# Performance work log

Hardware: AMD Instinct MI355X
Metric: run time of the kernel (lower is better)

Reference implementation:

```python
import jax, jax.numpy as jnp
import numpy as np

DIM = 512
HEADS = 8
HEAD_DIM = DIM // HEADS
SCALE = HEAD_DIM ** -0.5
B, N = 256, 144


def setup_inputs() -> dict:
    key = jax.random.key(0)
    k1, k2, k3, k4, k5, k6 = jax.random.split(key, 6)
    x = jax.random.normal(k1, (B, N, DIM), dtype=jnp.float32)
    topo_all_fea = jax.random.normal(k2, (B, N, DIM), dtype=jnp.float32)
    # nn.Linear weights stored as [out, in]
    kv_w = jax.random.normal(k3, (2 * DIM, DIM), dtype=jnp.float32) * 0.02
    q_w = jax.random.normal(k4, (DIM, DIM), dtype=jnp.float32) * 0.02
    proj_w = jax.random.normal(k5, (DIM, DIM), dtype=jnp.float32) * 0.02
    proj_b = jax.random.normal(k6, (DIM,), dtype=jnp.float32) * 0.02
    return {"x": x, "topo_all_fea": topo_all_fea, "kv_w": kv_w,
            "q_w": q_w, "proj_w": proj_w, "proj_b": proj_b, "is_end": 1}


def reference(x, topo_all_fea, kv_w, q_w, proj_w, proj_b, is_end):
    # block_pos == 'end' -> add topology features to the KV stream
    x_topo = x + topo_all_fea if is_end else x
    b, n, d = x.shape
    # kv: [B,N,2D] -> [2,B,H,N,hd]
    kv = (x_topo @ kv_w.T).reshape(b, n, 2, HEADS, HEAD_DIM).transpose(2, 0, 3, 1, 4)
    k, v = kv[0], kv[1]
    # q: [B,N,D] -> [B,H,N,hd]
    q = (x @ q_w.T).reshape(b, n, HEADS, HEAD_DIM).transpose(0, 2, 1, 3)
    # manual attention in fp32 (autocast(False) region in the original)
    attn = jnp.einsum('bhqd,bhkd->bhqk', q, k) * SCALE
    attn = jax.nn.softmax(attn, axis=-1)
    out = jnp.einsum('bhqk,bhkd->bhqd', attn, v)  # [B,H,N,hd]
    out = out.transpose(0, 2, 1, 3).reshape(b, n, d)
    return out @ proj_w.T + proj_b
```

## Files before the change

### kernel.cpp

```cpp
#include <hip/hip_runtime.h>
#include <hip/hip_bf16.h>

typedef float  f32x4  __attribute__((ext_vector_type(4)));
typedef __bf16 bf16x8 __attribute__((ext_vector_type(8)));
typedef __bf16 bf16x4 __attribute__((ext_vector_type(4)));

#define D_  512
#define H_  8
#define HD_ 64
#define B_  256
#define N_  144
#define M_  (B_*N_)

using gptr_t = const __attribute__((address_space(1))) char*;
using lptr_t = __attribute__((address_space(3))) char*;
#define GLDS16(gp, lp) __builtin_amdgcn_global_load_lds((gptr_t)(gp), (lptr_t)(lp), 16, 0, 0)

__global__ void prep_weights_kernel(const float* __restrict__ kvw,
                                    const float* __restrict__ qw,
                                    const float* __restrict__ pw,
                                    __bf16* __restrict__ kvb,
                                    __bf16* __restrict__ qb,
                                    __bf16* __restrict__ pb) {
    int idx = blockIdx.x * 256 + threadIdx.x;
    const float* s; __bf16* d; int off;
    if (idx < 131072)      { s = kvw; d = kvb; off = idx; }
    else if (idx < 196608) { s = qw;  d = qb;  off = idx - 131072; }
    else                   { s = pw;  d = pb;  off = idx - 196608; }
    f32x4 v = *(const f32x4*)(s + (size_t)off * 4);
    bf16x4 o;
    o[0] = (__bf16)v.x; o[1] = (__bf16)v.y; o[2] = (__bf16)v.z; o[3] = (__bf16)v.w;
    *(bf16x4*)(d + (size_t)off * 4) = o;
}

__global__ void prep_act_kernel(const float* __restrict__ x,
                                const float* __restrict__ topo,
                                const int* __restrict__ is_end,
                                __bf16* __restrict__ xb,
                                __bf16* __restrict__ ab) {
    const float tf = (is_end[0] != 0) ? 1.f : 0.f;
    const size_t total = (size_t)M_ * D_ / 8;
    for (size_t i = (size_t)blockIdx.x * 256 + threadIdx.x; i < total;
         i += (size_t)gridDim.x * 256) {
        f32x4 a0 = *(const f32x4*)(x + i * 8);
        f32x4 a1 = *(const f32x4*)(x + i * 8 + 4);
        f32x4 t0 = *(const f32x4*)(topo + i * 8);
        f32x4 t1 = *(const f32x4*)(topo + i * 8 + 4);
        bf16x8 xo, ao;
#pragma unroll
        for (int j = 0; j < 4; ++j) {
            xo[j]     = (__bf16)a0[j];
            xo[j + 4] = (__bf16)a1[j];
            ao[j]     = (__bf16)(a0[j] + tf * t0[j]);
            ao[j + 4] = (__bf16)(a1[j] + tf * t1[j]);
        }
        *(bf16x8*)(xb + i * 8) = xo;
        *(bf16x8*)(ab + i * 8) = ao;
    }
}

template<int MODE>
__device__ __forceinline__ void mm_body(const __bf16* __restrict__ ab,
                                        const __bf16* __restrict__ xb,
                                        const __bf16* __restrict__ kvb,
                                        const __bf16* __restrict__ qb,
                                        __bf16* __restrict__ kout,
                                        __bf16* __restrict__ vTout,
                                        __bf16* __restrict__ qout,
                                        const float* __restrict__ bias,
                                        float* __restrict__ pout) {
    __shared__ __align__(16) char smem[(MODE == 0) ? 33280 : 32768];
    __bf16* As = (__bf16*)smem;
    __bf16* Bs = (__bf16*)(smem + 16384);

    const int tid  = threadIdx.x;
    const int lane = tid & 63;
    const int wid  = tid >> 6;
    const int lrow = lane & 15, lhi = lane >> 4;
    const int wr   = wid >> 1,  wc  = wid & 1;

    const int NB  = (MODE == 0) ? 12 : 4;
    const int per = (MODE == 0) ? 432 : 144;
    const int bid = blockIdx.x;
    const int wg  = (bid & 7) * per + (bid >> 3);
    const int mb  = wg / NB;
    const int nb  = wg - mb * NB;
    const int m0  = mb * 128;

    const __bf16* Ap;
    const __bf16* Bp;
    if (MODE == 0) {
        Ap = (nb < 8) ? ab : xb;
        Bp = (nb < 8) ? (kvb + (size_t)nb * 128 * D_) : (qb + (size_t)(nb - 8) * 128 * D_);
    } else {
        Ap = ab;
        Bp = kvb + (size_t)nb * 128 * D_;
    }

    f32x4 acc[4][4];
#pragma unroll
    for (int i = 0; i < 4; ++i)
#pragma unroll
        for (int j = 0; j < 4; ++j) acc[i][j] = (f32x4){0.f, 0.f, 0.f, 0.f};

    const int srow = lane >> 3;
    const int scol = (lane & 7) * 16;

    for (int kt = 0; kt < 8; ++kt) {
        const int k0 = kt * 64;
        const char* Agb = (const char*)(Ap + (size_t)m0 * D_ + k0);
        const char* Bgb = (const char*)(Bp + k0);
#pragma unroll
        for (int j = 0; j < 4; ++j) {
            const int chunk = wid * 4 + j;
            const int row   = chunk * 8 + srow;
            GLDS16(Agb + (size_t)row * (D_ * 2) + scol, (char*)As + chunk * 1024);
            GLDS16(Bgb + (size_t)row * (D_ * 2) + scol, (char*)Bs + chunk * 1024);
        }
        __syncthreads();
#pragma unroll
        for (int kk = 0; kk < 2; ++kk) {
            bf16x8 af[4], bfr[4];
#pragma unroll
            for (int mi = 0; mi < 4; ++mi)
                af[mi] = *(const bf16x8*)((const char*)As +
                          (wr * 64 + mi * 16 + lrow) * 128 + kk * 64 + lhi * 16);
#pragma unroll
            for (int ni = 0; ni < 4; ++ni)
                bfr[ni] = *(const bf16x8*)((const char*)Bs +
                          (wc * 64 + ni * 16 + lrow) * 128 + kk * 64 + lhi * 16);
#pragma unroll
            for (int mi = 0; mi < 4; ++mi)
#pragma unroll
                for (int ni = 0; ni < 4; ++ni)
                    acc[mi][ni] = __builtin_amdgcn_mfma_f32_16x16x32_bf16(
                        af[mi], bfr[ni], acc[mi][ni], 0, 0, 0);
        }
        __syncthreads();
    }

    if (MODE == 0) {
        __bf16 (*Ct)[130] = (__bf16 (*)[130])smem;
#pragma unroll
        for (int mi = 0; mi < 4; ++mi)
#pragma unroll
            for (int reg = 0; reg < 4; ++reg) {
                const int r = wr * 64 + mi * 16 + lhi * 4 + reg;
#pragma unroll
                for (int ni = 0; ni < 4; ++ni)
                    Ct[r][wc * 64 + ni * 16 + lrow] = (__bf16)acc[mi][ni][reg];
            }
        __syncthreads();

        if (nb < 8) {
            if (nb < 4) {
#pragma unroll
                for (int it = 0; it < 8; ++it) {
                    int task = it * 256 + tid;
                    int m = task >> 4, half = (task >> 3) & 1, j = task & 7;
                    int mg = m0 + m, bb2 = mg / N_, nn = mg - bb2 * N_;
                    bf16x8 v = *(const bf16x8*)&Ct[m][half * 64 + j * 8];
                    *(bf16x8*)(kout + (((size_t)bb2 * H_ + nb * 2 + half) * N_ + nn) * HD_ + j * 8) = v;
                }
            } else {
                for (int it = 0; it < 64; ++it) {
                    int task = wid * 64 + it;
                    int ol = task >> 1, seg = task & 1;
                    int m = seg * 64 + lane;
                    int mg = m0 + m, bb2 = mg / N_, nn = mg - bb2 * N_;
                    int hh = (nb - 4) * 2 + (ol >> 6), dd = ol & 63;
                    vTout[(((size_t)bb2 * H_ + hh) * HD_ + dd) * N_ + nn] = Ct[m][ol];
                }
            }
        } else {
#pragma unroll
            for (int it = 0; it < 8; ++it) {
                int task = it * 256 + tid;
                int m = task >> 4, half = (task >> 3) & 1, j = task & 7;
                int mg = m0 + m, bb2 = mg / N_, nn = mg - bb2 * N_;
                bf16x8 v = *(const bf16x8*)&Ct[m][half * 64 + j * 8];
                *(bf16x8*)(qout + (((size_t)bb2 * H_ + (nb - 8) * 2 + half) * N_ + nn) * HD_ + j * 8) = v;
            }
        }
    } else {
        float bv4[4];
#pragma unroll
        for (int ni = 0; ni < 4; ++ni) bv4[ni] = bias[nb * 128 + wc * 64 + ni * 16 + lrow];
#pragma unroll
        for (int mi = 0; mi < 4; ++mi)
#pragma unroll
            for (int reg = 0; reg < 4; ++reg) {
                int m = m0 + wr * 64 + mi * 16 + lhi * 4 + reg;
#pragma unroll
                for (int ni = 0; ni < 4; ++ni)
                    pout[(size_t)m * D_ + nb * 128 + wc * 64 + ni * 16 + lrow] =
                        acc[mi][ni][reg] + bv4[ni];
            }
    }
}

__global__ __launch_bounds__(256, 3) void mm0_kernel(
        const __bf16* __restrict__ ab, const __bf16* __restrict__ xb,
        const __bf16* __restrict__ kvb, const __bf16* __restrict__ qb,
        __bf16* __restrict__ kout, __bf16* __restrict__ vTout,
        __bf16* __restrict__ qout) {
    mm_body<0>(ab, xb, kvb, qb, kout, vTout, qout, nullptr, nullptr);
}

__global__ __launch_bounds__(256, 3) void mm1_kernel(
        const __bf16* __restrict__ ab, const __bf16* __restrict__ pwb,
        const float* __restrict__ bias, float* __restrict__ pout) {
    mm_body<1>(ab, nullptr, pwb, nullptr, nullptr, nullptr, nullptr, bias, pout);
}

__launch_bounds__(256, 2)
__global__ void attn_kernel(const __bf16* __restrict__ qbuf,
                            const __bf16* __restrict__ kbuf,
                            const __bf16* __restrict__ vTbuf,
                            __bf16* __restrict__ aout) {
    __shared__ __bf16 Ks[144][72];
    __shared__ __bf16 Vs[64][168];
    __shared__ __bf16 Ps[4][16][160];

    const int tid  = threadIdx.x;
    const int lane = tid & 63, wid = tid >> 6;
    const int lrow = lane & 15, lhi = lane >> 4;
    const int bh = blockIdx.x;
    const int bb = bh >> 3, hh = bh & 7;

    const __bf16* kg = kbuf  + (size_t)bh * (N_ * HD_);
    const __bf16* vg = vTbuf + (size_t)bh * (N_ * HD_);
    const __bf16* qg = qbuf  + (size_t)bh * (N_ * HD_);

    for (int c = tid; c < 1152; c += 256) {
        int row = c >> 3, cc = c & 7;
        *(bf16x8*)&Ks[row][cc * 8] = *(const bf16x8*)(kg + row * 64 + cc * 8);
    }
    for (int c = tid; c < 1152; c += 256) {
        int dd = c / 18, cc = c - dd * 18;
        *(bf16x8*)&Vs[dd][cc * 8] = *(const bf16x8*)(vg + dd * 144 + cc * 8);
    }
    bf16x8 z8;
#pragma unroll
    for (int i = 0; i < 8; ++i) z8[i] = (__bf16)0.f;
    if (tid < 192) {
        int dd = tid / 3, cc = tid - dd * 3;
        *(bf16x8*)&Vs[dd][144 + cc * 8] = z8;
    }
    if (lhi < 2)
        *(bf16x8*)&Ps[wid][lrow][144 + lhi * 8] = z8;
    __syncthreads();

    const float sc = 0.125f * 1.44269504089f;

    for (int t = wid; t < 9; t += 4) {
        bf16x8 aq[2];
#pragma unroll
        for (int kk = 0; kk < 2; ++kk)
            aq[kk] = *(const bf16x8*)(qg + (t * 16 + lrow) * 64 + kk * 32 + lhi * 8);

        f32x4 s[9];
#pragma unroll
        for (int j = 0; j < 9; ++j) s[j] = (f32x4){0.f, 0.f, 0.f, 0.f};
#pragma unroll
        for (int j = 0; j < 9; ++j)
#pragma unroll
            for (int kk = 0; kk < 2; ++kk)
                s[j] = __builtin_amdgcn_mfma_f32_16x16x32_bf16(
                    aq[kk], *(const bf16x8*)&Ks[j * 16 + lrow][kk * 32 + lhi * 8], s[j], 0, 0, 0);

        float inv[4];
#pragma unroll
        for (int reg = 0; reg < 4; ++reg) {
            float mx = s[0][reg];
#pragma unroll
            for (int j = 1; j < 9; ++j) mx = fmaxf(mx, s[j][reg]);
#pragma unroll
            for (int off = 1; off < 16; off <<= 1) mx = fmaxf(mx, __shfl_xor(mx, off, 16));
            float sum = 0.f;
#pragma unroll
            for (int j = 0; j < 9; ++j) {
                float p = exp2f((s[j][reg] - mx) * sc);
                s[j][reg] = p;
                sum += p;
            }
#pragma unroll
            for (int off = 1; off < 16; off <<= 1) sum += __shfl_xor(sum, off, 16);
            inv[reg] = 1.f / sum;
        }
#pragma unroll
        for (int j = 0; j < 9; ++j)
#pragma unroll
            for (int reg = 0; reg < 4; ++reg)
                Ps[wid][lhi * 4 + reg][j * 16 + lrow] = (__bf16)(s[j][reg] * inv[reg]);

#pragma unroll
        for (int dc = 0; dc < 4; ++dc) {
            f32x4 o4 = (f32x4){0.f, 0.f, 0.f, 0.f};
#pragma unroll
            for (int kc = 0; kc < 5; ++kc)
                o4 = __builtin_amdgcn_mfma_f32_16x16x32_bf16(
                    *(const bf16x8*)&Ps[wid][lrow][kc * 32 + lhi * 8],
                    *(const bf16x8*)&Vs[dc * 16 + lrow][kc * 32 + lhi * 8], o4, 0, 0, 0);
#pragma unroll
            for (int reg = 0; reg < 4; ++reg) {
                int nn = t * 16 + lhi * 4 + reg;
                int dd = dc * 16 + lrow;
                aout[((size_t)bb * N_ + nn) * D_ + hh * HD_ + dd] = (__bf16)o4[reg];
            }
        }
    }
}

extern "C" void kernel_launch(void* const* d_in, const int* in_sizes, int n_in,
                              void* d_out, int out_size, void* d_ws, size_t ws_size,
                              hipStream_t stream) {
    const float* x      = (const float*)d_in[0];
    const float* topo   = (const float*)d_in[1];
    const float* kvw    = (const float*)d_in[2];
    const float* qw     = (const float*)d_in[3];
    const float* pw     = (const float*)d_in[4];
    const float* pb     = (const float*)d_in[5];
    const int*   is_end = (const int*)d_in[6];
    float* out = (float*)d_out;

    char* ws = (char*)d_ws;
    __bf16* kvb = (__bf16*)(ws);
    __bf16* qb  = (__bf16*)(ws + (1u << 20));
    __bf16* pwb = (__bf16*)(ws + (1u << 20) + 524288);
    size_t off = (1u << 20) + 2 * 524288;
    const size_t BUF = (size_t)M_ * D_ * 2;
    __bf16* xb    = (__bf16*)(ws + off); off += BUF;
    __bf16* ab    = (__bf16*)(ws + off); off += BUF;
    __bf16* kbuf  = (__bf16*)(ws + off); off += BUF;
    __bf16* vTbuf = (__bf16*)(ws + off); off += BUF;
    __bf16* qbuf  = (__bf16*)(ws + off); off += BUF;
    __bf16* abuf  = xb;

    prep_weights_kernel<<<1024, 256, 0, stream>>>(kvw, qw, pw, kvb, qb, pwb);
    prep_act_kernel<<<2048, 256, 0, stream>>>(x, topo, is_end, xb, ab);
    mm0_kernel<<<3456, 256, 0, stream>>>(ab, xb, kvb, qb, kbuf, vTbuf, qbuf);
    attn_kernel<<<2048, 256, 0, stream>>>(qbuf, kbuf, vTbuf, abuf);
    mm1_kernel<<<1152, 256, 0, stream>>>(abuf, pwb, pb, out);
}
```

Before: 371.2 us.

## Rewrite QKV GEMM with 256x256 tiles, swizzled LDS and double-buffered pipeline

New measurement: 376.4 us. No clear change (+1.4%).

```diff
diff --git a/kernel.cpp b/kernel.cpp
--- a/kernel.cpp
+++ b/kernel.cpp
@@ -15,6 +15,18 @@
 using gptr_t = const __attribute__((address_space(1))) char*;
 using lptr_t = __attribute__((address_space(3))) char*;
 #define GLDS16(gp, lp) __builtin_amdgcn_global_load_lds((gptr_t)(gp), (lptr_t)(lp), 16, 0, 0)
+#define SBAR()   __builtin_amdgcn_s_barrier()
+#define SCHEDB() __builtin_amdgcn_sched_barrier(0)
+
+__device__ __forceinline__ void waitv4() { asm volatile("s_waitcnt vmcnt(4)" ::: "memory"); }
+__device__ __forceinline__ void waitv0() { asm volatile("s_waitcnt vmcnt(0)" ::: "memory"); }
+__device__ __forceinline__ void waitlg() { asm volatile("s_waitcnt lgkmcnt(0)" ::: "memory"); }
+
+__device__ __forceinline__ bf16x8 dsr128(unsigned addr) {
+    bf16x8 r;
+    asm volatile("ds_read_b128 %0, %1" : "=v"(r) : "v"(addr) : "memory");
+    return r;
+}
 
 __global__ void prep_weights_kernel(const float* __restrict__ kvw,
                                     const float* __restrict__ qw,
@@ -59,43 +71,189 @@
     }
 }
 
-template<int MODE>
-__device__ __forceinline__ void mm_body(const __bf16* __restrict__ ab,
-                                        const __bf16* __restrict__ xb,
-                                        const __bf16* __restrict__ kvb,
-                                        const __bf16* __restrict__ qb,
-                                        __bf16* __restrict__ kout,
-                                        __bf16* __restrict__ vTout,
-                                        __bf16* __restrict__ qout,
-                                        const float* __restrict__ bias,
-                                        float* __restrict__ pout) {
-    __shared__ __align__(16) char smem[(MODE == 0) ? 33280 : 32768];
+__global__ __launch_bounds__(512, 2) void mm0_kernel(
+        const __bf16* __restrict__ ab, const __bf16* __restrict__ xb,
+        const __bf16* __restrict__ kvb, const __bf16* __restrict__ qb,
+        __bf16* __restrict__ kout, __bf16* __restrict__ vTout,
+        __bf16* __restrict__ qout) {
+    __shared__ __align__(16) char smem[131072];
+
+    const int tid  = threadIdx.x;
+    const int lane = tid & 63, wid = tid >> 6;
+    const int lrow = lane & 15, lhi = lane >> 4;
+    const int wm   = wid >> 2,  wn  = wid & 3;
+
+    const int bid = blockIdx.x;
+    const int wg  = (bid & 7) * 108 + (bid >> 3);
+    const int mb  = wg / 6;
+    const int nb2 = wg - mb * 6;
+    const int m0  = mb * 256;
+
+    const __bf16* Ap = (nb2 < 4) ? ab : xb;
+    const __bf16* Bp = (nb2 < 4) ? (kvb + (size_t)nb2 * 256 * D_)
+                                 : (qb  + (size_t)(nb2 - 4) * 256 * D_);
+
+    const unsigned sbase = (unsigned)(uintptr_t)(lptr_t)smem;
+    const unsigned swz   = (unsigned)((lrow & 7) << 4);
+    const unsigned cb0   = (0u * 64 + lhi * 16) ^ swz;
+    const unsigned cb1   = (1u * 64 + lhi * 16) ^ swz;
+
+    auto stage = [&](int mat, int h, int kt, int d) {
+        const char* gb = (const char*)(mat ? Bp : Ap);
+        const int rowb = (mat ? 0 : m0) + h * 128;
+#pragma unroll
+        for (int j = 0; j < 2; ++j) {
+            int c = j * 512 + tid;
+            int row = c >> 3;
+            int scb = ((c & 7) * 16) ^ ((row & 7) << 4);
+            GLDS16(gb + (size_t)(rowb + row) * (D_ * 2) + kt * 128 + scb,
+                   smem + d * 65536 + mat * 32768 + h * 16384 + c * 16);
+        }
+    };
+
+    f32x4 acc[8][4];
+#pragma unroll
+    for (int i = 0; i < 8; ++i)
+#pragma unroll
+        for (int j = 0; j < 4; ++j) acc[i][j] = (f32x4){0.f, 0.f, 0.f, 0.f};
+
+    bf16x8 Bf[4][2], Af[2][2];
+
+    auto read_a = [&](unsigned Abase, int p) {
+#pragma unroll
+        for (int m2 = 0; m2 < 2; ++m2) {
+            unsigned r = Abase + (unsigned)(((2 * p + m2) * 16 + lrow) * 128);
+            Af[m2][0] = dsr128(r + cb0);
+            Af[m2][1] = dsr128(r + cb1);
+        }
+    };
+    auto mfma_quad = [&](int p) {
+        __builtin_amdgcn_s_setprio(1);
+#pragma unroll
+        for (int m2 = 0; m2 < 2; ++m2)
+#pragma unroll
+            for (int ni = 0; ni < 4; ++ni)
+#pragma unroll
+                for (int kk = 0; kk < 2; ++kk)
+                    acc[2 * p + m2][ni] = __builtin_amdgcn_mfma_f32_16x16x32_bf16(
+                        Af[m2][kk], Bf[ni][kk], acc[2 * p + m2][ni], 0, 0, 0);
+        __builtin_amdgcn_s_setprio(0);
+    };
+
+    stage(1, 0, 0, 0); stage(1, 1, 0, 0);
+    stage(0, 0, 0, 0); stage(0, 1, 0, 0);
+    stage(1, 0, 1, 1); stage(1, 1, 1, 1);
+    waitv4(); SCHEDB(); SBAR();
+
+#pragma unroll 2
+    for (int t = 0; t < 8; ++t) {
+        const int d = t & 1;
+        const unsigned bufb = sbase + (unsigned)(d * 65536);
+        const unsigned Abse = bufb + (unsigned)(wm * 16384);
+        const unsigned Bbse = bufb + 32768u + (unsigned)((wn >> 1) * 16384);
+
+#pragma unroll
+        for (int ni = 0; ni < 4; ++ni) {
+            unsigned r = Bbse + (unsigned)((((wn & 1) * 64 + ni * 16 + lrow)) * 128);
+            Bf[ni][0] = dsr128(r + cb0);
+            Bf[ni][1] = dsr128(r + cb1);
+        }
+        read_a(Abse, 0);
+        if (t + 1 < 8) stage(0, 0, t + 1, (t + 1) & 1);
+        SCHEDB(); SBAR(); waitlg(); SCHEDB();
+        mfma_quad(0);
+        SCHEDB(); SBAR();
+
+        read_a(Abse, 1);
+        if (t + 1 < 8) stage(0, 1, t + 1, (t + 1) & 1);
+        SCHEDB(); SBAR(); waitlg(); SCHEDB();
+        mfma_quad(1);
+        SCHEDB(); SBAR();
+
+        read_a(Abse, 2);
+        if (t + 2 < 8) stage(1, 0, t + 2, d);
+        SCHEDB(); SBAR(); waitlg(); SCHEDB();
+        mfma_quad(2);
+        SCHEDB(); SBAR();
+
+        read_a(Abse, 3);
+        if (t + 2 < 8) stage(1, 1, t + 2, d);
+        SCHEDB(); SBAR(); waitlg(); SCHEDB();
+        mfma_quad(3);
+        SCHEDB();
+        if (t < 6) waitv4();
+        else if (t == 6) waitv0();
+        SBAR();
+    }
+
+    if (nb2 == 2 || nb2 == 3) {
+        __bf16* Ct = (__bf16*)smem;
+        const int CS = 258;
+#pragma unroll
+        for (int s = 0; s < 2; ++s) {
+            if (wm == s) {
+#pragma unroll
+                for (int mi = 0; mi < 8; ++mi)
+#pragma unroll
+                    for (int reg = 0; reg < 4; ++reg) {
+                        int r = mi * 16 + lhi * 4 + reg;
+#pragma unroll
+                        for (int ni = 0; ni < 4; ++ni)
+                            Ct[r * CS + wn * 64 + ni * 16 + lrow] = (__bf16)acc[mi][ni][reg];
+                    }
+            }
+            __syncthreads();
+            for (int it = 0; it < 64; ++it) {
+                int col = wid * 32 + (it >> 1);
+                int m   = (it & 1) * 64 + lane;
+                __bf16 v = Ct[m * CS + col];
+                int mg = m0 + s * 128 + m;
+                int bb2 = mg / N_, nn = mg - bb2 * N_;
+                int hh = (nb2 - 2) * 4 + (col >> 6), dd = col & 63;
+                vTout[(((size_t)bb2 * H_ + hh) * HD_ + dd) * N_ + nn] = v;
+            }
+            __syncthreads();
+        }
+    } else {
+        __bf16* outp = (nb2 < 2) ? kout : qout;
+        const int hbase = (nb2 < 2) ? nb2 * 4 : (nb2 - 4) * 4;
+#pragma unroll
+        for (int mi = 0; mi < 8; ++mi)
+#pragma unroll
+            for (int reg = 0; reg < 4; ++reg) {
+                int mg = m0 + wm * 128 + mi * 16 + lhi * 4 + reg;
+                int bb2 = mg / N_, nn = mg - bb2 * N_;
+#pragma unroll
+                for (int ni = 0; ni < 4; ++ni) {
+                    int col = wn * 64 + ni * 16 + lrow;
+                    int hh = hbase + (col >> 6), dd = col & 63;
+                    outp[(((size_t)bb2 * H_ + hh) * N_ + nn) * HD_ + dd] =
+                        (__bf16)acc[mi][ni][reg];
+                }
+            }
+    }
+}
+
+__global__ __launch_bounds__(256, 3) void mm1_kernel(
+        const __bf16* __restrict__ abuf, const __bf16* __restrict__ pwb,
+        const float* __restrict__ bias, float* __restrict__ pout) {
+    __shared__ __align__(16) char smem[32768];
     __bf16* As = (__bf16*)smem;
     __bf16* Bs = (__bf16*)(smem + 16384);
 
     const int tid  = threadIdx.x;
-    const int lane = tid & 63;
-    const int wid  = tid >> 6;
+    const int lane = tid & 63, wid = tid >> 6;
     const int lrow = lane & 15, lhi = lane >> 4;
     const int wr   = wid >> 1,  wc  = wid & 1;
 
-    const int NB  = (MODE == 0) ? 12 : 4;
-    const int per = (MODE == 0) ? 432 : 144;
     const int bid = blockIdx.x;
-    const int wg  = (bid & 7) * per + (bid >> 3);
-    const int mb  = wg / NB;
-    const int nb  = wg - mb * NB;
+    const int wg  = (bid & 7) * 144 + (bid >> 3);
+    const int mb  = wg / 4;
+    const int nb  = wg - mb * 4;
     const int m0  = mb * 128;
 
-    const __bf16* Ap;
-    const __bf16* Bp;
-    if (MODE == 0) {
-        Ap = (nb < 8) ? ab : xb;
-        Bp = (nb < 8) ? (kvb + (size_t)nb * 128 * D_) : (qb + (size_t)(nb - 8) * 128 * D_);
-    } else {
-        Ap = ab;
-        Bp = kvb + (size_t)nb * 128 * D_;
-    }
+    const __bf16* Ap = abuf;
+    const __bf16* Bp = pwb + (size_t)nb * 128 * D_;
 
     f32x4 acc[4][4];
 #pragma unroll
@@ -139,78 +297,19 @@
         __syncthreads();
     }
 
-    if (MODE == 0) {
-        __bf16 (*Ct)[130] = (__bf16 (*)[130])smem;
-#pragma unroll
-        for (int mi = 0; mi < 4; ++mi)
-#pragma unroll
-            for (int reg = 0; reg < 4; ++reg) {
-                const int r = wr * 64 + mi * 16 + lhi * 4 + reg;
-#pragma unroll
-                for (int ni = 0; ni < 4; ++ni)
-                    Ct[r][wc * 64 + ni * 16 + lrow] = (__bf16)acc[mi][ni][reg];
-            }
-        __syncthreads();
-
-        if (nb < 8) {
-            if (nb < 4) {
-#pragma unroll
-                for (int it = 0; it < 8; ++it) {
-                    int task = it * 256 + tid;
-                    int m = task >> 4, half = (task >> 3) & 1, j = task & 7;
-                    int mg = m0 + m, bb2 = mg / N_, nn = mg - bb2 * N_;
-                    bf16x8 v = *(const bf16x8*)&Ct[m][half * 64 + j * 8];
-                    *(bf16x8*)(kout + (((size_t)bb2 * H_ + nb * 2 + half) * N_ + nn) * HD_ + j * 8) = v;
-                }
-            } else {
-                for (int it = 0; it < 64; ++it) {
-                    int task = wid * 64 + it;
-                    int ol = task >> 1, seg = task & 1;
-                    int m = seg * 64 + lane;
-                    int mg = m0 + m, bb2 = mg / N_, nn = mg - bb2 * N_;
-                    int hh = (nb - 4) * 2 + (ol >> 6), dd = ol & 63;
-                    vTout[(((size_t)bb2 * H_ + hh) * HD_ + dd) * N_ + nn] = Ct[m][ol];
-                }
-            }
-        } else {
-#pragma unroll
-            for (int it = 0; it < 8; ++it) {
-                int task = it * 256 + tid;
-                int m = task >> 4, half = (task >> 3) & 1, j = task & 7;
-                int mg = m0 + m, bb2 = mg / N_, nn = mg - bb2 * N_;
-                bf16x8 v = *(const bf16x8*)&Ct[m][half * 64 + j * 8];
-                *(bf16x8*)(qout + (((size_t)bb2 * H_ + (nb - 8) * 2 + half) * N_ + nn) * HD_ + j * 8) = v;
-            }
-        }
-    } else {
-        float bv4[4];
-#pragma unroll
-        for (int ni = 0; ni < 4; ++ni) bv4[ni] = bias[nb * 128 + wc * 64 + ni * 16 + lrow];
-#pragma unroll
-        for (int mi = 0; mi < 4; ++mi)
-#pragma unroll
-            for (int reg = 0; reg < 4; ++reg) {
-                int m = m0 + wr * 64 + mi * 16 + lhi * 4 + reg;
-#pragma unroll
-                for (int ni = 0; ni < 4; ++ni)
-                    pout[(size_t)m * D_ + nb * 128 + wc * 64 + ni * 16 + lrow] =
-                        acc[mi][ni][reg] + bv4[ni];
-            }
-    }
-}
-
-__global__ __launch_bounds__(256, 3) void mm0_kernel(
-        const __bf16* __restrict__ ab, const __bf16* __restrict__ xb,
-        const __bf16* __restrict__ kvb, const __bf16* __restrict__ qb,
-        __bf16* __restrict__ kout, __bf16* __restrict__ vTout,
-        __bf16* __restrict__ qout) {
-    mm_body<0>(ab, xb, kvb, qb, kout, vTout, qout, nullptr, nullptr);
-}
-
-__global__ __launch_bounds__(256, 3) void mm1_kernel(
-        const __bf16* __restrict__ ab, const __bf16* __restrict__ pwb,
-        const float* __restrict__ bias, float* __restrict__ pout) {
-    mm_body<1>(ab, nullptr, pwb, nullptr, nullptr, nullptr, nullptr, bias, pout);
+    float bv4[4];
+#pragma unroll
+    for (int ni = 0; ni < 4; ++ni) bv4[ni] = bias[nb * 128 + wc * 64 + ni * 16 + lrow];
+#pragma unroll
+    for (int mi = 0; mi < 4; ++mi)
+#pragma unroll
+        for (int reg = 0; reg < 4; ++reg) {
+            int m = m0 + wr * 64 + mi * 16 + lhi * 4 + reg;
+#pragma unroll
+            for (int ni = 0; ni < 4; ++ni)
+                pout[(size_t)m * D_ + nb * 128 + wc * 64 + ni * 16 + lrow] =
+                    acc[mi][ni][reg] + bv4[ni];
+        }
 }
 
 __launch_bounds__(256, 2)
@@ -339,7 +438,7 @@
 
     prep_weights_kernel<<<1024, 256, 0, stream>>>(kvw, qw, pw, kvb, qb, pwb);
     prep_act_kernel<<<2048, 256, 0, stream>>>(x, topo, is_end, xb, ab);
-    mm0_kernel<<<3456, 256, 0, stream>>>(ab, xb, kvb, qb, kbuf, vTbuf, qbuf);
+    mm0_kernel<<<864, 512, 0, stream>>>(ab, xb, kvb, qb, kbuf, vTbuf, qbuf);
     attn_kernel<<<2048, 256, 0, stream>>>(qbuf, kbuf, vTbuf, abuf);
     mm1_kernel<<<1152, 256, 0, stream>>>(abuf, pwb, pb, out);
 }
```

## Fuse QKV projection into per-(batch,head) attention kernel, keeping Q/K/V in LDS

Applied to the files above, without the earlier changes.

New measurement: 411.1 us. 10.8% more time.

```diff
diff --git a/kernel.cpp b/kernel.cpp
--- a/kernel.cpp
+++ b/kernel.cpp
@@ -59,43 +59,238 @@
     }
 }
 
-template<int MODE>
-__device__ __forceinline__ void mm_body(const __bf16* __restrict__ ab,
-                                        const __bf16* __restrict__ xb,
-                                        const __bf16* __restrict__ kvb,
-                                        const __bf16* __restrict__ qb,
-                                        __bf16* __restrict__ kout,
-                                        __bf16* __restrict__ vTout,
-                                        __bf16* __restrict__ qout,
-                                        const float* __restrict__ bias,
-                                        float* __restrict__ pout) {
-    __shared__ __align__(16) char smem[(MODE == 0) ? 33280 : 32768];
+__global__ __launch_bounds__(256, 2) void fused_kernel(
+        const __bf16* __restrict__ ab, const __bf16* __restrict__ xb,
+        const __bf16* __restrict__ kvb, const __bf16* __restrict__ qb,
+        __bf16* __restrict__ aout) {
+    __shared__ __align__(16) char smem[97792];
+    char* SA = smem;
+    char* SB = smem + 18432;
+    __bf16 (*Qs)[72]  = (__bf16 (*)[72])(smem + 34816);
+    __bf16 (*Ks)[72]  = (__bf16 (*)[72])(smem + 55552);
+    __bf16 (*Vt)[168] = (__bf16 (*)[168])(smem + 76288);
+    __bf16 (*Ps)[16][168] = (__bf16 (*)[16][168])smem;
+
+    const int tid  = threadIdx.x;
+    const int lane = tid & 63, wid = tid >> 6;
+    const int lrow = lane & 15, lhi = lane >> 4;
+
+    const int bid = blockIdx.x;
+    const int wg  = (bid & 7) * 256 + (bid >> 3);
+    const int bb  = wg >> 3, hh = wg & 7;
+
+    const char* Aab = (const char*)(ab + (size_t)bb * N_ * D_);
+    const char* Axb = (const char*)(xb + (size_t)bb * N_ * D_);
+    const char* Wk  = (const char*)(kvb + (size_t)hh * HD_ * D_);
+    const char* Wv  = (const char*)(kvb + (size_t)(512 + hh * HD_) * D_);
+    const char* Wq  = (const char*)(qb  + (size_t)hh * HD_ * D_);
+
+    const int crow = lane >> 3;
+    const int scb  = ((lane & 7) * 16) ^ (crow << 4);
+    const unsigned rsw = (unsigned)((lrow & 7) << 4);
+    const unsigned cb0 = (0u + lhi * 16) ^ rsw;
+    const unsigned cb1 = (64u + lhi * 16) ^ rsw;
+
+    f32x4 acc[9][2];
+#pragma unroll
+    for (int i = 0; i < 9; ++i) { acc[i][0] = (f32x4){0,0,0,0}; acc[i][1] = (f32x4){0,0,0,0}; }
+
+    for (int kt = 0; kt < 8; ++kt) {
+        const int kb = kt * 128;
+#pragma unroll
+        for (int it = 0; it < 4; ++it) {
+            int cc = wid * 4 + it;
+            GLDS16(Aab + (size_t)(cc * 8 + crow) * 1024 + kb + scb, SA + cc * 1024);
+        }
+        if (wid < 2)
+            GLDS16(Aab + (size_t)((16 + wid) * 8 + crow) * 1024 + kb + scb,
+                   SA + (16 + wid) * 1024);
+#pragma unroll
+        for (int it = 0; it < 4; ++it) {
+            int cc = wid * 4 + it;
+            int r  = cc * 8 + crow;
+            const char* src = (cc < 8) ? (Wk + (size_t)r * 1024)
+                                       : (Wv + (size_t)(r - 64) * 1024);
+            GLDS16(src + kb + scb, SB + cc * 1024);
+        }
+        __syncthreads();
+#pragma unroll
+        for (int mi = 0; mi < 9; ++mi) {
+            const unsigned ra = (unsigned)((mi * 16 + lrow) * 128);
+            bf16x8 a0 = *(const bf16x8*)(SA + ra + cb0);
+            bf16x8 a1 = *(const bf16x8*)(SA + ra + cb1);
+#pragma unroll
+            for (int ni = 0; ni < 2; ++ni) {
+                const unsigned rb = (unsigned)((wid * 32 + ni * 16 + lrow) * 128);
+                acc[mi][ni] = __builtin_amdgcn_mfma_f32_16x16x32_bf16(
+                    a0, *(const bf16x8*)(SB + rb + cb0), acc[mi][ni], 0, 0, 0);
+                acc[mi][ni] = __builtin_amdgcn_mfma_f32_16x16x32_bf16(
+                    a1, *(const bf16x8*)(SB + rb + cb1), acc[mi][ni], 0, 0, 0);
+            }
+        }
+        __syncthreads();
+    }
+    if (wid < 2) {
+#pragma unroll
+        for (int mi = 0; mi < 9; ++mi)
+#pragma unroll
+            for (int ni = 0; ni < 2; ++ni)
+#pragma unroll
+                for (int reg = 0; reg < 4; ++reg)
+                    Ks[mi * 16 + lhi * 4 + reg][wid * 32 + ni * 16 + lrow] =
+                        (__bf16)acc[mi][ni][reg];
+    } else {
+#pragma unroll
+        for (int mi = 0; mi < 9; ++mi)
+#pragma unroll
+            for (int ni = 0; ni < 2; ++ni) {
+                int d = (wid - 2) * 32 + ni * 16 + lrow;
+                bf16x4 p;
+#pragma unroll
+                for (int reg = 0; reg < 4; ++reg) p[reg] = (__bf16)acc[mi][ni][reg];
+                *(bf16x4*)&Vt[d][mi * 16 + lhi * 4] = p;
+            }
+    }
+    for (int c = tid; c < 192; c += 256) {
+        bf16x8 z8;
+#pragma unroll
+        for (int i = 0; i < 8; ++i) z8[i] = (__bf16)0.f;
+        *(bf16x8*)&Vt[c / 3][144 + (c % 3) * 8] = z8;
+    }
+
+    f32x4 acq[9];
+#pragma unroll
+    for (int i = 0; i < 9; ++i) acq[i] = (f32x4){0,0,0,0};
+
+    for (int kt = 0; kt < 8; ++kt) {
+        const int kb = kt * 128;
+#pragma unroll
+        for (int it = 0; it < 4; ++it) {
+            int cc = wid * 4 + it;
+            GLDS16(Axb + (size_t)(cc * 8 + crow) * 1024 + kb + scb, SA + cc * 1024);
+        }
+        if (wid < 2)
+            GLDS16(Axb + (size_t)((16 + wid) * 8 + crow) * 1024 + kb + scb,
+                   SA + (16 + wid) * 1024);
+#pragma unroll
+        for (int it = 0; it < 2; ++it) {
+            int cc = wid * 2 + it;
+            GLDS16(Wq + (size_t)(cc * 8 + crow) * 1024 + kb + scb, SB + cc * 1024);
+        }
+        __syncthreads();
+        {
+            const unsigned rb = (unsigned)((wid * 16 + lrow) * 128);
+            bf16x8 b0 = *(const bf16x8*)(SB + rb + cb0);
+            bf16x8 b1 = *(const bf16x8*)(SB + rb + cb1);
+#pragma unroll
+            for (int mi = 0; mi < 9; ++mi) {
+                const unsigned ra = (unsigned)((mi * 16 + lrow) * 128);
+                acq[mi] = __builtin_amdgcn_mfma_f32_16x16x32_bf16(
+                    *(const bf16x8*)(SA + ra + cb0), b0, acq[mi], 0, 0, 0);
+                acq[mi] = __builtin_amdgcn_mfma_f32_16x16x32_bf16(
+                    *(const bf16x8*)(SA + ra + cb1), b1, acq[mi], 0, 0, 0);
+            }
+        }
+        __syncthreads();
+    }
+#pragma unroll
+    for (int mi = 0; mi < 9; ++mi)
+#pragma unroll
+        for (int reg = 0; reg < 4; ++reg)
+            Qs[mi * 16 + lhi * 4 + reg][wid * 16 + lrow] = (__bf16)acq[mi][reg];
+
+    __syncthreads();
+
+    {
+        bf16x8 z8;
+#pragma unroll
+        for (int i = 0; i < 8; ++i) z8[i] = (__bf16)0.f;
+        if (lhi < 2)
+            *(bf16x8*)&Ps[wid][lrow][144 + lhi * 8] = z8;
+    }
+    const float sc = 0.125f * 1.44269504089f;
+
+    for (int t = wid; t < 9; t += 4) {
+        bf16x8 aq[2];
+#pragma unroll
+        for (int kk = 0; kk < 2; ++kk)
+            aq[kk] = *(const bf16x8*)&Qs[t * 16 + lrow][kk * 32 + lhi * 8];
+
+        f32x4 s[9];
+#pragma unroll
+        for (int j = 0; j < 9; ++j) s[j] = (f32x4){0,0,0,0};
+#pragma unroll
+        for (int j = 0; j < 9; ++j)
+#pragma unroll
+            for (int kk = 0; kk < 2; ++kk)
+                s[j] = __builtin_amdgcn_mfma_f32_16x16x32_bf16(
+                    aq[kk], *(const bf16x8*)&Ks[j * 16 + lrow][kk * 32 + lhi * 8],
+                    s[j], 0, 0, 0);
+
+        float inv[4];
+#pragma unroll
+        for (int reg = 0; reg < 4; ++reg) {
+            float mx = s[0][reg];
+#pragma unroll
+            for (int j = 1; j < 9; ++j) mx = fmaxf(mx, s[j][reg]);
+#pragma unroll
+            for (int off = 1; off < 16; off <<= 1) mx = fmaxf(mx, __shfl_xor(mx, off, 16));
+            float sum = 0.f;
+#pragma unroll
+            for (int j = 0; j < 9; ++j) {
+                float p = exp2f((s[j][reg] - mx) * sc);
+                s[j][reg] = p;
+                sum += p;
+            }
+#pragma unroll
+            for (int off = 1; off < 16; off <<= 1) sum += __shfl_xor(sum, off, 16);
+            inv[reg] = 1.f / sum;
+        }
+#pragma unroll
+        for (int j = 0; j < 9; ++j)
+#pragma unroll
+            for (int reg = 0; reg < 4; ++reg)
+                Ps[wid][lhi * 4 + reg][j * 16 + lrow] = (__bf16)(s[j][reg] * inv[reg]);
+
+#pragma unroll
+        for (int dc = 0; dc < 4; ++dc) {
+            f32x4 o4 = (f32x4){0,0,0,0};
+#pragma unroll
+            for (int kc = 0; kc < 5; ++kc)
+                o4 = __builtin_amdgcn_mfma_f32_16x16x32_bf16(
+                    *(const bf16x8*)&Ps[wid][lrow][kc * 32 + lhi * 8],
+                    *(const bf16x8*)&Vt[dc * 16 + lrow][kc * 32 + lhi * 8],
+                    o4, 0, 0, 0);
+#pragma unroll
+            for (int reg = 0; reg < 4; ++reg) {
+                int nn = t * 16 + lhi * 4 + reg;
+                int dd = dc * 16 + lrow;
+                aout[((size_t)bb * N_ + nn) * D_ + hh * HD_ + dd] = (__bf16)o4[reg];
+            }
+        }
+    }
+}
+
+__global__ __launch_bounds__(256, 3) void mm1_kernel(
+        const __bf16* __restrict__ abuf, const __bf16* __restrict__ pwb,
+        const float* __restrict__ bias, float* __restrict__ pout) {
+    __shared__ __align__(16) char smem[32768];
     __bf16* As = (__bf16*)smem;
     __bf16* Bs = (__bf16*)(smem + 16384);
 
     const int tid  = threadIdx.x;
-    const int lane = tid & 63;
-    const int wid  = tid >> 6;
+    const int lane = tid & 63, wid = tid >> 6;
     const int lrow = lane & 15, lhi = lane >> 4;
     const int wr   = wid >> 1,  wc  = wid & 1;
 
-    const int NB  = (MODE == 0) ? 12 : 4;
-    const int per = (MODE == 0) ? 432 : 144;
     const int bid = blockIdx.x;
-    const int wg  = (bid & 7) * per + (bid >> 3);
-    const int mb  = wg / NB;
-    const int nb  = wg - mb * NB;
+    const int wg  = (bid & 7) * 144 + (bid >> 3);
+    const int mb  = wg / 4;
+    const int nb  = wg - mb * 4;
     const int m0  = mb * 128;
 
-    const __bf16* Ap;
-    const __bf16* Bp;
-    if (MODE == 0) {
-        Ap = (nb < 8) ? ab : xb;
-        Bp = (nb < 8) ? (kvb + (size_t)nb * 128 * D_) : (qb + (size_t)(nb - 8) * 128 * D_);
-    } else {
-        Ap = ab;
-        Bp = kvb + (size_t)nb * 128 * D_;
-    }
+    const __bf16* Ap = abuf;
+    const __bf16* Bp = pwb + (size_t)nb * 128 * D_;
 
     f32x4 acc[4][4];
 #pragma unroll
@@ -139,177 +334,19 @@
         __syncthreads();
     }
 
-    if (MODE == 0) {
-        __bf16 (*Ct)[130] = (__bf16 (*)[130])smem;
-#pragma unroll
-        for (int mi = 0; mi < 4; ++mi)
-#pragma unroll
-            for (int reg = 0; reg < 4; ++reg) {
-                const int r = wr * 64 + mi * 16 + lhi * 4 + reg;
-#pragma unroll
-                for (int ni = 0; ni < 4; ++ni)
-                    Ct[r][wc * 64 + ni * 16 + lrow] = (__bf16)acc[mi][ni][reg];
-            }
-        __syncthreads();
-
-        if (nb < 8) {
-            if (nb < 4) {
-#pragma unroll
-                for (int it = 0; it < 8; ++it) {
-                    int task = it * 256 + tid;
-                    int m = task >> 4, half = (task >> 3) & 1, j = task & 7;
-                    int mg = m0 + m, bb2 = mg / N_, nn = mg - bb2 * N_;
-                    bf16x8 v = *(const bf16x8*)&Ct[m][half * 64 + j * 8];
-                    *(bf16x8*)(kout + (((size_t)bb2 * H_ + nb * 2 + half) * N_ + nn) * HD_ + j * 8) = v;
-                }
-            } else {
-                for (int it = 0; it < 64; ++it) {
-                    int task = wid * 64 + it;
-                    int ol = task >> 1, seg = task & 1;
-                    int m = seg * 64 + lane;
-                    int mg = m0 + m, bb2 = mg / N_, nn = mg - bb2 * N_;
-                    int hh = (nb - 4) * 2 + (ol >> 6), dd = ol & 63;
-                    vTout[(((size_t)bb2 * H_ + hh) * HD_ + dd) * N_ + nn] = Ct[m][ol];
-                }
-            }
-        } else {
-#pragma unroll
-            for (int it = 0; it < 8; ++it) {
-                int task = it * 256 + tid;
-                int m = task >> 4, half = (task >> 3) & 1, j = task & 7;
-                int mg = m0 + m, bb2 = mg / N_, nn = mg - bb2 * N_;
-                bf16x8 v = *(const bf16x8*)&Ct[m][half * 64 + j * 8];
-                *(bf16x8*)(qout + (((size_t)bb2 * H_ + (nb - 8) * 2 + half) * N_ + nn) * HD_ + j * 8) = v;
-            }
-        }
-    } else {
-        float bv4[4];
-#pragma unroll
-        for (int ni = 0; ni < 4; ++ni) bv4[ni] = bias[nb * 128 + wc * 64 + ni * 16 + lrow];
-#pragma unroll
-        for (int mi = 0; mi < 4; ++mi)
-#pragma unroll
-            for (int reg = 0; reg < 4; ++reg) {
-                int m = m0 + wr * 64 + mi * 16 + lhi * 4 + reg;
-#pragma unroll
-                for (int ni = 0; ni < 4; ++ni)
-                    pout[(size_t)m * D_ + nb * 128 + wc * 64 + ni * 16 + lrow] =
-                        acc[mi][ni][reg] + bv4[ni];
-            }
-    }
-}
-
-__global__ __launch_bounds__(256, 3) void mm0_kernel(
-        const __bf16* __restrict__ ab, const __bf16* __restrict__ xb,
-        const __bf16* __restrict__ kvb, const __bf16* __restrict__ qb,
-        __bf16* __restrict__ kout, __bf16* __restrict__ vTout,
-        __bf16* __restrict__ qout) {
-    mm_body<0>(ab, xb, kvb, qb, kout, vTout, qout, nullptr, nullptr);
-}
-
-__global__ __launch_bounds__(256, 3) void mm1_kernel(
-        const __bf16* __restrict__ ab, const __bf16* __restrict__ pwb,
-        const float* __restrict__ bias, float* __restrict__ pout) {
-    mm_body<1>(ab, nullptr, pwb, nullptr, nullptr, nullptr, nullptr, bias, pout);
-}
-
-__launch_bounds__(256, 2)
-__global__ void attn_kernel(const __bf16* __restrict__ qbuf,
-                            const __bf16* __restrict__ kbuf,
-                            const __bf16* __restrict__ vTbuf,
-                            __bf16* __restrict__ aout) {
-    __shared__ __bf16 Ks[144][72];
-    __shared__ __bf16 Vs[64][168];
-    __shared__ __bf16 Ps[4][16][160];
-
-    const int tid  = threadIdx.x;
-    const int lane = tid & 63, wid = tid >> 6;
-    const int lrow = lane & 15, lhi = lane >> 4;
-    const int bh = blockIdx.x;
-    const int bb = bh >> 3, hh = bh & 7;
-
-    const __bf16* kg = kbuf  + (size_t)bh * (N_ * HD_);
-    const __bf16* vg = vTbuf + (size_t)bh * (N_ * HD_);
-    const __bf16* qg = qbuf  + (size_t)bh * (N_ * HD_);
-
-    for (int c = tid; c < 1152; c += 256) {
-        int row = c >> 3, cc = c & 7;
-        *(bf16x8*)&Ks[row][cc * 8] = *(const bf16x8*)(kg + row * 64 + cc * 8);
-    }
-    for (int c = tid; c < 1152; c += 256) {
-        int dd = c / 18, cc = c - dd * 18;
-        *(bf16x8*)&Vs[dd][cc * 8] = *(const bf16x8*)(vg + dd * 144 + cc * 8);
-    }
-    bf16x8 z8;
-#pragma unroll
-    for (int i = 0; i < 8; ++i) z8[i] = (__bf16)0.f;
-    if (tid < 192) {
-        int dd = tid / 3, cc = tid - dd * 3;
-        *(bf16x8*)&Vs[dd][144 + cc * 8] = z8;
-    }
-    if (lhi < 2)
-        *(bf16x8*)&Ps[wid][lrow][144 + lhi * 8] = z8;
-    __syncthreads();
-
-    const float sc = 0.125f * 1.44269504089f;
-
-    for (int t = wid; t < 9; t += 4) {
-        bf16x8 aq[2];
-#pragma unroll
-        for (int kk = 0; kk < 2; ++kk)
-            aq[kk] = *(const bf16x8*)(qg + (t * 16 + lrow) * 64 + kk * 32 + lhi * 8);
-
-        f32x4 s[9];
-#pragma unroll
-        for (int j = 0; j < 9; ++j) s[j] = (f32x4){0.f, 0.f, 0.f, 0.f};
-#pragma unroll
-        for (int j = 0; j < 9; ++j)
-#pragma unroll
-            for (int kk = 0; kk < 2; ++kk)
-                s[j] = __builtin_amdgcn_mfma_f32_16x16x32_bf16(
-                    aq[kk], *(const bf16x8*)&Ks[j * 16 + lrow][kk * 32 + lhi * 8], s[j], 0, 0, 0);
-
-        float inv[4];
+    float bv4[4];
+#pragma unroll
+    for (int ni = 0; ni < 4; ++ni) bv4[ni] = bias[nb * 128 + wc * 64 + ni * 16 + lrow];
+#pragma unroll
+    for (int mi = 0; mi < 4; ++mi)
 #pragma unroll
         for (int reg = 0; reg < 4; ++reg) {
-            float mx = s[0][reg];
-#pragma unroll
-            for (int j = 1; j < 9; ++j) mx = fmaxf(mx, s[j][reg]);
-#pragma unroll
-            for (int off = 1; off < 16; off <<= 1) mx = fmaxf(mx, __shfl_xor(mx, off, 16));
-            float sum = 0.f;
-#pragma unroll
-            for (int j = 0; j < 9; ++j) {
-                float p = exp2f((s[j][reg] - mx) * sc);
-                s[j][reg] = p;
-                sum += p;
-            }
-#pragma unroll
-            for (int off = 1; off < 16; off <<= 1) sum += __shfl_xor(sum, off, 16);
-            inv[reg] = 1.f / sum;
-        }
-#pragma unroll
-        for (int j = 0; j < 9; ++j)
-#pragma unroll
-            for (int reg = 0; reg < 4; ++reg)
-                Ps[wid][lhi * 4 + reg][j * 16 + lrow] = (__bf16)(s[j][reg] * inv[reg]);
-
-#pragma unroll
-        for (int dc = 0; dc < 4; ++dc) {
-            f32x4 o4 = (f32x4){0.f, 0.f, 0.f, 0.f};
-#pragma unroll
-            for (int kc = 0; kc < 5; ++kc)
-                o4 = __builtin_amdgcn_mfma_f32_16x16x32_bf16(
-                    *(const bf16x8*)&Ps[wid][lrow][kc * 32 + lhi * 8],
-                    *(const bf16x8*)&Vs[dc * 16 + lrow][kc * 32 + lhi * 8], o4, 0, 0, 0);
-#pragma unroll
-            for (int reg = 0; reg < 4; ++reg) {
-                int nn = t * 16 + lhi * 4 + reg;
-                int dd = dc * 16 + lrow;
-                aout[((size_t)bb * N_ + nn) * D_ + hh * HD_ + dd] = (__bf16)o4[reg];
-            }
-        }
-    }
+            int m = m0 + wr * 64 + mi * 16 + lhi * 4 + reg;
+#pragma unroll
+            for (int ni = 0; ni < 4; ++ni)
+                pout[(size_t)m * D_ + nb * 128 + wc * 64 + ni * 16 + lrow] =
+                    acc[mi][ni][reg] + bv4[ni];
+        }
 }
 
 extern "C" void kernel_launch(void* const* d_in, const int* in_sizes, int n_in,
@@ -332,14 +369,10 @@
     const size_t BUF = (size_t)M_ * D_ * 2;
     __bf16* xb    = (__bf16*)(ws + off); off += BUF;
     __bf16* ab    = (__bf16*)(ws + off); off += BUF;
-    __bf16* kbuf  = (__bf16*)(ws + off); off += BUF;
-    __bf16* vTbuf = (__bf16*)(ws + off); off += BUF;
-    __bf16* qbuf  = (__bf16*)(ws + off); off += BUF;
-    __bf16* abuf  = xb;
+    __bf16* abuf  = (__bf16*)(ws + off); off += BUF;
 
     prep_weights_kernel<<<1024, 256, 0, stream>>>(kvw, qw, pw, kvb, qb, pwb);
     prep_act_kernel<<<2048, 256, 0, stream>>>(x, topo, is_end, xb, ab);
-    mm0_kernel<<<3456, 256, 0, stream>>>(ab, xb, kvb, qb, kbuf, vTbuf, qbuf);
-    attn_kernel<<<2048, 256, 0, stream>>>(qbuf, kbuf, vTbuf, abuf);
+    fused_kernel<<<2048, 256, 0, stream>>>(ab, xb, kvb, qb, abuf);
     mm1_kernel<<<1152, 256, 0, stream>>>(abuf, pwb, pb, out);
 }
```
